# Optimization experiments

Hardware: AMD Instinct MI355X
Metric: run time of the kernel (lower is better)

Reference implementation:

```python
import jax, jax.numpy as jnp
import numpy as np

BN_SCALE = 1.0 / np.sqrt(1.0 + 1e-5)  # eval BatchNorm with running stats (0,1), gamma=1, beta=0


def fps(xyz, npoint):
    """Farthest point sampling. xyz: [B,N,3] -> int32 indices [B,npoint]. First pick is index 0 (as in pointnet2 CUDA)."""
    xyz = jax.lax.stop_gradient(xyz)  # output is integer indices; non-differentiable
    B, N, _ = xyz.shape

    def step(carry, _):
        dist, last = carry
        p = jnp.take_along_axis(xyz, last[:, None, None], axis=1)  # [B,1,3]
        d = jnp.sum((xyz - p) ** 2, axis=-1)                        # [B,N]
        dist = jnp.minimum(dist, d)
        nxt = jnp.argmax(dist, axis=-1).astype(jnp.int32)
        return (dist, nxt), nxt

    dist0 = jnp.full((B, N), 1e10, dtype=jnp.float32)
    first = jnp.zeros((B,), dtype=jnp.int32)
    _, rest = jax.lax.scan(step, (dist0, first), None, length=npoint - 1)  # [npoint-1, B]
    return jnp.concatenate([first[None, :], rest], axis=0).T  # [B, npoint]


def ball_query(xyz, new_xyz, radius, nsample):
    """For each center pick first nsample point indices with squared dist < radius^2; pad with first hit."""
    xyz = jax.lax.stop_gradient(xyz)
    new_xyz = jax.lax.stop_gradient(new_xyz)
    # expanded squared distance avoids materializing [B,S,N,3]
    d2 = (jnp.sum(new_xyz ** 2, -1)[:, :, None] + jnp.sum(xyz ** 2, -1)[:, None, :]
          - 2.0 * jnp.einsum('bsc,bnc->bsn', new_xyz, xyz))  # [B,S,N]
    N = xyz.shape[1]
    key = jnp.where(d2 < radius * radius, jnp.arange(N, dtype=jnp.int32)[None, None, :], N)
    idx = jnp.sort(key, axis=-1)[..., :nsample]          # first hits in index order
    return jnp.where(idx == N, idx[..., :1], idx)        # pad misses with first hit (center is always a hit)


_gather = jax.vmap(lambda p, i: p[i])  # points [N,C], idx [...] -> [..., C], batched over B


def _mlp(h, params):
    # pointwise Conv2d(1x1) + eval-BN + ReLU stack
    for w, b in params:
        h = jax.nn.relu((h @ w + b) * BN_SCALE)
    return h


def _sa(xyz, feats, npoint, nsample, radius, params):
    ci = fps(xyz, npoint)                               # [B,S]
    new_xyz = _gather(xyz, ci)                          # [B,S,3]
    idx = ball_query(xyz, new_xyz, radius, nsample)     # [B,S,K]
    gx = _gather(xyz, idx) - new_xyz[:, :, None, :]     # centered grouped xyz [B,S,K,3]
    h = jnp.concatenate([gx, _gather(feats, idx)], -1)  # [B,S,K,3+C]
    h = _mlp(h, params)
    return new_xyz, jnp.max(h, axis=2)                  # max-pool over neighbors -> [B,S,Cout]


def pointnetpp_forward(x, w1_0, b1_0, w1_1, b1_1, w1_2, b1_2,
                       w2_0, b2_0, w2_1, b2_1, w2_2, b2_2,
                       w3_0, b3_0, w3_1, b3_1, w3_2, b3_2, fc_w, fc_b):
    B0, NO, NP, C = x.shape
    pc = x.reshape(B0 * NO, NP, C)
    xyz, feats = pc[..., :3], pc[..., 3:]
    xyz, feats = _sa(xyz, feats, 32, 32, 0.2, [(w1_0, b1_0), (w1_1, b1_1), (w1_2, b1_2)])
    xyz, feats = _sa(xyz, feats, 16, 32, 0.4, [(w2_0, b2_0), (w2_1, b2_1), (w2_2, b2_2)])
    # group-all SA: no FPS, no centering (pointnet2 GroupAll)
    h = jnp.concatenate([xyz, feats], -1)[:, None]       # [B,1,N,3+C]
    h = _mlp(h, [(w3_0, b3_0), (w3_1, b3_1), (w3_2, b3_2)])
    g = jnp.max(h, axis=2).reshape(h.shape[0], -1)       # [B,768]
    out = g @ fc_w + fc_b                                # final Linear(768,768)
    return out.reshape(B0, NO, -1)                       # dropout = identity (eval / no_grad inference)


def setup_inputs():
    key = jax.random.key(0)
    ks = jax.random.split(key, 16)
    dims = {'w1_0': (6, 64), 'w1_1': (64, 64), 'w1_2': (64, 128),
            'w2_0': (131, 128), 'w2_1': (128, 128), 'w2_2': (128, 256),
            'w3_0': (259, 256), 'w3_1': (256, 512), 'w3_2': (512, 768),
            'fc_w': (768, 768)}
    inp = {'x': jax.random.normal(ks[0], (32, 64, 1024, 6), dtype=jnp.float32)}
    for i, (name, shp) in enumerate(dims.items()):
        inp[name] = 0.05 * jax.random.normal(ks[i + 1], shp, dtype=jnp.float32)
        bname = 'fc_b' if name == 'fc_w' else name.replace('w', 'b', 1)
        inp[bname] = jnp.zeros((shp[1],), dtype=jnp.float32)
    return inp


def reference(x, w1_0, b1_0, w1_1, b1_1, w1_2, b1_2,
              w2_0, b2_0, w2_1, b2_1, w2_2, b2_2,
              w3_0, b3_0, w3_1, b3_1, w3_2, b3_2, fc_w, fc_b):
    return pointnetpp_forward(x, w1_0, b1_0, w1_1, b1_1, w1_2, b1_2,
                              w2_0, b2_0, w2_1, b2_1, w2_2, b2_2,
                              w3_0, b3_0, w3_1, b3_1, w3_2, b3_2, fc_w, fc_b)
```

## Files before the change

### kernel.cpp

```cpp
#include <hip/hip_runtime.h>
#include <math.h>

#define BN_SCALE 0.999995000037499687f
#define NPTS 1024
#define NB   2048

typedef __attribute__((ext_vector_type(8))) short bh8;
typedef __attribute__((ext_vector_type(4))) float f32x4;

__device__ __forceinline__ float sq3(float x, float y, float z) {
  return __fadd_rn(__fadd_rn(__fmul_rn(x, x), __fmul_rn(y, y)), __fmul_rn(z, z));
}

__device__ __forceinline__ short bf16hi(float v) {
  unsigned u = __float_as_uint(v);
  unsigned r = (u + 0x7FFFu + ((u >> 16) & 1u)) >> 16;
  return (short)r;
}
__device__ __forceinline__ float bf16tof(short s) {
  unsigned u = ((unsigned)(unsigned short)s) << 16;
  return __uint_as_float(u);
}
__device__ __forceinline__ void bf16split(float v, short& hi, short& lo) {
  hi = bf16hi(v);
  lo = bf16hi(v - bf16tof(hi));
}

__global__ __launch_bounds__(256) void k_fps1(const float* __restrict__ x,
                                              float* __restrict__ nxyz1) {
  int b = blockIdx.x;
  const float* cloud = x + (size_t)b * NPTS * 6;
  __shared__ float px[NPTS], py[NPTS], pz[NPTS], dist[NPTS];
  __shared__ float wv_s[4];
  __shared__ int   wi_s[4];
  __shared__ int   last_s;
  int t = threadIdx.x;
  for (int i = t; i < NPTS; i += 256) {
    px[i] = cloud[i * 6 + 0];
    py[i] = cloud[i * 6 + 1];
    pz[i] = cloud[i * 6 + 2];
    dist[i] = 1e10f;
  }
  __syncthreads();
  if (t == 0) {
    nxyz1[(size_t)b * 96 + 0] = px[0];
    nxyz1[(size_t)b * 96 + 1] = py[0];
    nxyz1[(size_t)b * 96 + 2] = pz[0];
  }
  int last = 0;
  for (int s = 1; s < 32; ++s) {
    float lx = px[last], ly = py[last], lz = pz[last];
    float bv = -1.0f; int bi = NPTS;
    for (int i = t; i < NPTS; i += 256) {
      float dx = __fsub_rn(px[i], lx);
      float dy = __fsub_rn(py[i], ly);
      float dz = __fsub_rn(pz[i], lz);
      float d  = sq3(dx, dy, dz);
      float nd = fminf(dist[i], d);
      dist[i] = nd;
      if (nd > bv || (nd == bv && i < bi)) { bv = nd; bi = i; }
    }
    for (int off = 32; off; off >>= 1) {
      float ov = __shfl_down(bv, off);
      int   oi = __shfl_down(bi, off);
      if (ov > bv || (ov == bv && oi < bi)) { bv = ov; bi = oi; }
    }
    if ((t & 63) == 0) { wv_s[t >> 6] = bv; wi_s[t >> 6] = bi; }
    __syncthreads();
    if (t == 0) {
      for (int w = 1; w < 4; ++w)
        if (wv_s[w] > bv || (wv_s[w] == bv && wi_s[w] < bi)) { bv = wv_s[w]; bi = wi_s[w]; }
      last_s = bi;
      nxyz1[(size_t)b * 96 + s * 3 + 0] = px[bi];
      nxyz1[(size_t)b * 96 + s * 3 + 1] = py[bi];
      nxyz1[(size_t)b * 96 + s * 3 + 2] = pz[bi];
    }
    __syncthreads();
    last = last_s;
  }
}

__global__ __launch_bounds__(256) void k_bq1(const float* __restrict__ x,
                                             const float* __restrict__ nxyz1,
                                             int* __restrict__ idx1) {
  int c = blockIdx.x * 256 + threadIdx.x;
  if (c >= NB * 32) return;
  int b = c >> 5;
  const float* cloud = x + (size_t)b * NPTS * 6;
  float cx = nxyz1[c * 3 + 0], cy = nxyz1[c * 3 + 1], cz = nxyz1[c * 3 + 2];
  float sqc = sq3(cx, cy, cz);
  const float r2 = (float)(0.2 * 0.2);
  int hits = 0, fh = NPTS - 1;
  int* outp = idx1 + (size_t)c * 32;
  for (int i = 0; i < NPTS; ++i) {
    float ppx = cloud[i * 6 + 0], ppy = cloud[i * 6 + 1], ppz = cloud[i * 6 + 2];
    float sqp = sq3(ppx, ppy, ppz);
    float dt  = __fadd_rn(__fadd_rn(__fmul_rn(cx, ppx), __fmul_rn(cy, ppy)), __fmul_rn(cz, ppz));
    float d2  = __fsub_rn(__fadd_rn(sqc, sqp), __fmul_rn(2.0f, dt));
    if (d2 < r2) {
      if (hits == 0) fh = i;
      outp[hits] = i;
      if (++hits == 32) break;
    }
  }
  for (int j = hits; j < 32; ++j) outp[j] = fh;
}

__device__ __forceinline__ void prep_one(const float* __restrict__ src,
                                         short* __restrict__ dst,
                                         int q, int KT, int Kreal, int N) {
  int nt = q / (KT * 512);
  int r  = q - nt * (KT * 512);
  int kt = r >> 9;
  int e  = r & 511;
  int l = e >> 3, i = e & 7;
  int k = kt * 32 + ((l >> 4) << 3) + i;
  int col = nt * 16 + (l & 15);
  float v = (k < Kreal) ? src[(size_t)k * N + col] : 0.f;
  short hi, lo;
  bf16split(v, hi, lo);
  size_t base = ((size_t)(nt * KT + kt) * 2) * 512 + e;
  dst[base] = hi;
  dst[base + 512] = lo;
}

__global__ __launch_bounds__(256) void k_prep(const float* __restrict__ w0,
                                              const float* __restrict__ w1,
                                              const float* __restrict__ w2,
                                              short* __restrict__ wt0,
                                              short* __restrict__ wt1,
                                              short* __restrict__ wt2) {
  int p = blockIdx.x * 256 + threadIdx.x;
  const int S1 = 8 * 5 * 512, S2 = 8 * 4 * 512, S3 = 16 * 4 * 512;
  if (p < S1)                 prep_one(w0, wt0, p,           5, 131, 128);
  else if (p < S1 + S2)       prep_one(w1, wt1, p - S1,      4, 128, 128);
  else if (p < S1 + S2 + S3)  prep_one(w2, wt2, p - S1 - S2, 4, 128, 256);
}

__global__ __launch_bounds__(256) void k_prep1(const float* __restrict__ w0,
                                               const float* __restrict__ w1,
                                               const float* __restrict__ w2,
                                               short* __restrict__ wt0,
                                               short* __restrict__ wt1,
                                               short* __restrict__ wt2) {
  int p = blockIdx.x * 256 + threadIdx.x;
  const int S1 = 4 * 1 * 512, S2 = 4 * 2 * 512, S3 = 8 * 2 * 512;
  if (p < S1)                 prep_one(w0, wt0, p,           1, 6,  64);
  else if (p < S1 + S2)       prep_one(w1, wt1, p - S1,      2, 64, 64);
  else if (p < S1 + S2 + S3)  prep_one(w2, wt2, p - S1 - S2, 2, 64, 128);
}

__global__ __launch_bounds__(256) void k_prep3(const float* __restrict__ w0,
                                               const float* __restrict__ w1,
                                               const float* __restrict__ w2,
                                               const float* __restrict__ wf,
                                               short* __restrict__ wt0,
                                               short* __restrict__ wt1,
                                               short* __restrict__ wt2,
                                               short* __restrict__ wtf) {
  int p = blockIdx.x * 256 + threadIdx.x;
  const int S1 = 16 * 9 * 512;
  const int S2 = 32 * 8 * 512;
  const int S3 = 48 * 16 * 512;
  const int S4 = 48 * 24 * 512;
  if (p < S1)                      prep_one(w0, wt0, p,                9,  259, 256);
  else if (p < S1 + S2)            prep_one(w1, wt1, p - S1,           8,  256, 512);
  else if (p < S1 + S2 + S3)       prep_one(w2, wt2, p - S1 - S2,      16, 512, 768);
  else if (p < S1 + S2 + S3 + S4)  prep_one(wf, wtf, p - S1 - S2 - S3, 24, 768, 768);
}

template<int NTL, int KT, int PA, int MT>
__device__ __forceinline__ void mfma_gemm(const short* Ahi, const short* Alo,
                                          const short* __restrict__ wt,
                                          int w, int l, int lrow, int lk,
                                          f32x4 acc[][MT]) {
  for (int kt = 0; kt < KT; ++kt) {
    bh8 ahi[MT], alo[MT];
    #pragma unroll
    for (int mt = 0; mt < MT; ++mt) {
      int aoff = (mt * 16 + lrow) * PA + kt * 32 + lk;
      ahi[mt] = *(const bh8*)(Ahi + aoff);
      alo[mt] = *(const bh8*)(Alo + aoff);
    }
    #pragma unroll
    for (int ntl = 0; ntl < NTL; ++ntl) {
      int nt = w * NTL + ntl;
      bh8 bhi = *(const bh8*)(wt + (size_t)((nt * KT + kt) * 2 + 0) * 512 + l * 8);
      bh8 blo = *(const bh8*)(wt + (size_t)((nt * KT + kt) * 2 + 1) * 512 + l * 8);
      #pragma unroll
      for (int mt = 0; mt < MT; ++mt) {
        acc[ntl][mt] = __builtin_amdgcn_mfma_f32_16x16x32_bf16(ahi[mt], bhi, acc[ntl][mt], 0, 0, 0);
        acc[ntl][mt] = __builtin_amdgcn_mfma_f32_16x16x32_bf16(ahi[mt], blo, acc[ntl][mt], 0, 0, 0);
        acc[ntl][mt] = __builtin_amdgcn_mfma_f32_16x16x32_bf16(alo[mt], bhi, acc[ntl][mt], 0, 0, 0);
      }
    }
  }
}

template<int NTL, int PD, int MT>
__device__ __forceinline__ void epi_mid(f32x4 acc[][MT], const float* __restrict__ bias,
                                        short* Dhi, short* Dlo,
                                        int w, int lrow, int lhi4) {
  #pragma unroll
  for (int ntl = 0; ntl < NTL; ++ntl) {
    int col = (w * NTL + ntl) * 16 + lrow;
    float bv = bias[col];
    #pragma unroll
    for (int mt = 0; mt < MT; ++mt) {
      #pragma unroll
      for (int r = 0; r < 4; ++r) {
        int row = mt * 16 + lhi4 + r;
        float o = fmaxf((acc[ntl][mt][r] + bv) * BN_SCALE, 0.f);
        short hi, lo;
        bf16split(o, hi, lo);
        Dhi[row * PD + col] = hi;
        Dlo[row * PD + col] = lo;
      }
    }
  }
}

template<int NTL>
__device__ __forceinline__ void epi_max(f32x4 acc[][4], const float* __restrict__ bias,
                                        float* __restrict__ outA, float* __restrict__ outB,
                                        int w, int l, int lrow) {
  #pragma unroll
  for (int ntl = 0; ntl < NTL; ++ntl) {
    int col = (w * NTL + ntl) * 16 + lrow;
    float bv = bias[col];
    float m0 = 0.f, m1 = 0.f;
    #pragma unroll
    for (int mt = 0; mt < 4; ++mt) {
      float mm = 0.f;
      #pragma unroll
      for (int r = 0; r < 4; ++r)
        mm = fmaxf(mm, fmaxf((acc[ntl][mt][r] + bv) * BN_SCALE, 0.f));
      if (mt < 2) m0 = fmaxf(m0, mm); else m1 = fmaxf(m1, mm);
    }
    m0 = fmaxf(m0, __shfl_xor(m0, 16)); m0 = fmaxf(m0, __shfl_xor(m0, 32));
    m1 = fmaxf(m1, __shfl_xor(m1, 16)); m1 = fmaxf(m1, __shfl_xor(m1, 32));
    if (l < 16) {
      outA[col] = m0;
      outB[col] = m1;
    }
  }
}

__global__ __launch_bounds__(256) void k_sa1(const float* __restrict__ x,
                                             const float* __restrict__ nxyz1,
                                             const int* __restrict__ idx1,
                                             const short* __restrict__ wt0,
                                             const short* __restrict__ wt1,
                                             const short* __restrict__ wt2,
                                             const float* __restrict__ b0g,
                                             const float* __restrict__ b1g,
                                             const float* __restrict__ b2g,
                                             float* __restrict__ f1) {
  int c2 = blockIdx.x;
  int t  = threadIdx.x;
  __shared__ __align__(16) short lds[18432];
  __shared__ int pts[64];
  short* h0hi = lds;
  short* h0lo = lds + 4608;
  short* h1hi = lds + 9216;
  short* h1lo = lds + 13824;
  short* h2hi = lds;
  short* h2lo = lds + 4608;

  if (t < 64) {
    int g = t >> 5, samp = t & 31;
    pts[t] = idx1[(size_t)(c2 * 2 + g) * 32 + samp];
  }
  for (int j = t; j < 64 * 34; j += 256) {
    int s = j / 34, d = 6 + (j - s * 34);
    h0hi[s * 40 + d] = 0;
    h0lo[s * 40 + d] = 0;
  }
  __syncthreads();

  for (int j = t; j < 384; j += 256) {
    int s = j / 6, d = j - (j / 6) * 6;
    int g = s >> 5; int c = c2 * 2 + g; int b = c >> 5;
    int pt = pts[s];
    float v = x[((size_t)b * NPTS + pt) * 6 + d];
    if (d < 3) v -= nxyz1[(size_t)c * 3 + d];
    short hi, lo; bf16split(v, hi, lo);
    h0hi[s * 40 + d] = hi; h0lo[s * 40 + d] = lo;
  }
  __syncthreads();

  int l = t & 63, w = t >> 6;
  int lrow = l & 15;
  int lk   = (l >> 4) << 3;
  int lhi4 = (l >> 4) << 2;
  f32x4 zz = {0.f, 0.f, 0.f, 0.f};

  {
    f32x4 acc[1][4];
    #pragma unroll
    for (int j = 0; j < 4; ++j) acc[0][j] = zz;
    mfma_gemm<1, 1, 40, 4>(h0hi, h0lo, wt0, w, l, lrow, lk, acc);
    epi_mid<1, 72, 4>(acc, b0g, h1hi, h1lo, w, lrow, lhi4);
  }
  __syncthreads();
  {
    f32x4 acc[1][4];
    #pragma unroll
    for (int j = 0; j < 4; ++j) acc[0][j] = zz;
    mfma_gemm<1, 2, 72, 4>(h1hi, h1lo, wt1, w, l, lrow, lk, acc);
    epi_mid<1, 72, 4>(acc, b1g, h2hi, h2lo, w, lrow, lhi4);
  }
  __syncthreads();
  {
    f32x4 acc[2][4];
    #pragma unroll
    for (int i = 0; i < 2; ++i)
      #pragma unroll
      for (int j = 0; j < 4; ++j) acc[i][j] = zz;
    mfma_gemm<2, 2, 72, 4>(h2hi, h2lo, wt2, w, l, lrow, lk, acc);
    epi_max<2>(acc, b2g,
               f1 + (size_t)(c2 * 2 + 0) * 128,
               f1 + (size_t)(c2 * 2 + 1) * 128,
               w, l, lrow);
  }
}

__global__ __launch_bounds__(64) void k_fps2(const float* __restrict__ nxyz1,
                                             float* __restrict__ nxyz2) {
  int b = blockIdx.x;
  int t = threadIdx.x;
  const float* pts = nxyz1 + (size_t)b * 96;
  float ppx = 0.f, ppy = 0.f, ppz = 0.f, dist = -1.f;
  if (t < 32) { ppx = pts[t * 3]; ppy = pts[t * 3 + 1]; ppz = pts[t * 3 + 2]; dist = 1e10f; }
  if (t == 0) {
    nxyz2[(size_t)b * 48 + 0] = ppx;
    nxyz2[(size_t)b * 48 + 1] = ppy;
    nxyz2[(size_t)b * 48 + 2] = ppz;
  }
  int last = 0;
  for (int s = 1; s < 16; ++s) {
    float lx = __shfl(ppx, last), ly = __shfl(ppy, last), lz = __shfl(ppz, last);
    if (t < 32) {
      float dx = __fsub_rn(ppx, lx);
      float dy = __fsub_rn(ppy, ly);
      float dz = __fsub_rn(ppz, lz);
      dist = fminf(dist, sq3(dx, dy, dz));
    }
    float bv = dist; int bi = (t < 32) ? t : 1000;
    for (int off = 32; off; off >>= 1) {
      float ov = __shfl_xor(bv, off);
      int   oi = __shfl_xor(bi, off);
      if (ov > bv || (ov == bv && oi < bi)) { bv = ov; bi = oi; }
    }
    last = bi;
    float bx = __shfl(ppx, last), by = __shfl(ppy, last), bz = __shfl(ppz, last);
    if (t == 0) {
      nxyz2[(size_t)b * 48 + s * 3 + 0] = bx;
      nxyz2[(size_t)b * 48 + s * 3 + 1] = by;
      nxyz2[(size_t)b * 48 + s * 3 + 2] = bz;
    }
  }
}

__global__ __launch_bounds__(256) void k_bq2(const float* __restrict__ nxyz1,
                                             const float* __restrict__ nxyz2,
                                             int* __restrict__ idx2) {
  int c = blockIdx.x * 256 + threadIdx.x;
  if (c >= NB * 16) return;
  int b = c >> 4;
  const float* pts = nxyz1 + (size_t)b * 96;
  float cx = nxyz2[c * 3 + 0], cy = nxyz2[c * 3 + 1], cz = nxyz2[c * 3 + 2];
  float sqc = sq3(cx, cy, cz);
  const float r2 = (float)(0.4 * 0.4);
  int hits = 0, fh = 31;
  int* outp = idx2 + (size_t)c * 32;
  for (int i = 0; i < 32; ++i) {
    float ppx = pts[i * 3], ppy = pts[i * 3 + 1], ppz = pts[i * 3 + 2];
    float sqp = sq3(ppx, ppy, ppz);
    float dt  = __fadd_rn(__fadd_rn(__fmul_rn(cx, ppx), __fmul_rn(cy, ppy)), __fmul_rn(cz, ppz));
    float d2  = __fsub_rn(__fadd_rn(sqc, sqp), __fmul_rn(2.0f, dt));
    if (d2 < r2) { if (hits == 0) fh = i; outp[hits++] = i; }
  }
  for (int j = hits; j < 32; ++j) outp[j] = fh;
}

__global__ __launch_bounds__(256, 2) void k_sa2(const float* __restrict__ nxyz1,
                                                const float* __restrict__ nxyz2,
                                                const int* __restrict__ idx2,
                                                const float* __restrict__ f1,
                                                const short* __restrict__ wt0,
                                                const short* __restrict__ wt1,
                                                const short* __restrict__ wt2,
                                                const float* __restrict__ b0g,
                                                const float* __restrict__ b1g,
                                                const float* __restrict__ b2g,
                                                float* __restrict__ f2) {
  int c2 = blockIdx.x;
  int t  = threadIdx.x;
  __shared__ __align__(16) short lds[38912];
  __shared__ int pts[64];
  short* h0hi = lds;
  short* h0lo = lds + 10752;
  short* h1hi = lds + 21504;
  short* h1lo = lds + 30208;
  short* h2hi = lds;
  short* h2lo = lds + 10752;

  if (t < 64) {
    int g = t >> 5, samp = t & 31;
    pts[t] = idx2[(size_t)(c2 * 2 + g) * 32 + samp];
  }
  for (int j = t; j < 64 * 29; j += 256) {
    int s = j / 29, d = 131 + (j - s * 29);
    h0hi[s * 168 + d] = 0;
    h0lo[s * 168 + d] = 0;
  }
  __syncthreads();

  for (int j = t; j < 192; j += 256) {
    int s = j / 3, d = j - (j / 3) * 3;
    int g = s >> 5; int c = c2 * 2 + g; int b = c >> 4;
    int pt = pts[s];
    float v = nxyz1[((size_t)b * 32 + pt) * 3 + d] - nxyz2[(size_t)c * 3 + d];
    short hi, lo; bf16split(v, hi, lo);
    h0hi[s * 168 + d] = hi; h0lo[s * 168 + d] = lo;
  }
  for (int j = t; j < 2048; j += 256) {
    int s = j >> 5, d4 = j & 31;
    int g = s >> 5; int c = c2 * 2 + g; int b = c >> 4;
    int pt = pts[s];
    const float4 v4 = *reinterpret_cast<const float4*>(&f1[((size_t)b * 32 + pt) * 128 + d4 * 4]);
    int base = s * 168 + 3 + d4 * 4;
    short hi, lo;
    bf16split(v4.x, hi, lo); h0hi[base + 0] = hi; h0lo[base + 0] = lo;
    bf16split(v4.y, hi, lo); h0hi[base + 1] = hi; h0lo[base + 1] = lo;
    bf16split(v4.z, hi, lo); h0hi[base + 2] = hi; h0lo[base + 2] = lo;
    bf16split(v4.w, hi, lo); h0hi[base + 3] = hi; h0lo[base + 3] = lo;
  }
  __syncthreads();

  int l = t & 63, w = t >> 6;
  int lrow = l & 15;
  int lk   = (l >> 4) << 3;
  int lhi4 = (l >> 4) << 2;
  f32x4 zz = {0.f, 0.f, 0.f, 0.f};

  {
    f32x4 acc[2][4];
    #pragma unroll
    for (int i = 0; i < 2; ++i)
      #pragma unroll
      for (int j = 0; j < 4; ++j) acc[i][j] = zz;
    mfma_gemm<2, 5, 168, 4>(h0hi, h0lo, wt0, w, l, lrow, lk, acc);
    epi_mid<2, 136, 4>(acc, b0g, h1hi, h1lo, w, lrow, lhi4);
  }
  __syncthreads();
  {
    f32x4 acc[2][4];
    #pragma unroll
    for (int i = 0; i < 2; ++i)
      #pragma unroll
      for (int j = 0; j < 4; ++j) acc[i][j] = zz;
    mfma_gemm<2, 4, 136, 4>(h1hi, h1lo, wt1, w, l, lrow, lk, acc);
    epi_mid<2, 136, 4>(acc, b1g, h2hi, h2lo, w, lrow, lhi4);
  }
  __syncthreads();
  {
    f32x4 acc[4][4];
    #pragma unroll
    for (int i = 0; i < 4; ++i)
      #pragma unroll
      for (int j = 0; j < 4; ++j) acc[i][j] = zz;
    mfma_gemm<4, 4, 136, 4>(h2hi, h2lo, wt2, w, l, lrow, lk, acc);
    epi_max<4>(acc, b2g,
               f2 + (size_t)(c2 * 2 + 0) * 256,
               f2 + (size_t)(c2 * 2 + 1) * 256,
               w, l, lrow);
  }
}

__global__ __launch_bounds__(256) void k_mlp3(const float* __restrict__ nxyz2,
                                              const float* __restrict__ f2,
                                              const short* __restrict__ wt0,
                                              const short* __restrict__ wt1,
                                              const short* __restrict__ wt2,
                                              const float* __restrict__ b0g,
                                              const float* __restrict__ b1g,
                                              const float* __restrict__ b2g,
                                              short* __restrict__ ghi,
                                              short* __restrict__ glo) {
  int b = blockIdx.x;
  int t = threadIdx.x;
  __shared__ __align__(16) short lds[25088];
  short* h1hi = lds;
  short* h1lo = lds + 4224;
  short* h0hi = lds + 8448;
  short* h0lo = lds + 13184;
  short* h2hi = lds + 8448;
  short* h2lo = lds + 16768;

  for (int j = t; j < 16 * 29; j += 256) {
    int s = j / 29, d = 259 + (j - s * 29);
    h0hi[s * 296 + d] = 0;
    h0lo[s * 296 + d] = 0;
  }
  for (int j = t; j < 16 * 259; j += 256) {
    int s = j / 259, d = j - s * 259;
    float v = (d < 3) ? nxyz2[(size_t)b * 48 + s * 3 + d]
                      : f2[((size_t)b * 16 + s) * 256 + (d - 3)];
    short hi, lo; bf16split(v, hi, lo);
    h0hi[s * 296 + d] = hi;
    h0lo[s * 296 + d] = lo;
  }
  __syncthreads();

  int l = t & 63, w = t >> 6;
  int lrow = l & 15;
  int lk   = (l >> 4) << 3;
  int lhi4 = (l >> 4) << 2;
  f32x4 zz = {0.f, 0.f, 0.f, 0.f};

  {
    f32x4 acc[4][1];
    #pragma unroll
    for (int i = 0; i < 4; ++i) acc[i][0] = zz;
    mfma_gemm<4, 9, 296, 1>(h0hi, h0lo, wt0, w, l, lrow, lk, acc);
    epi_mid<4, 264, 1>(acc, b0g, h1hi, h1lo, w, lrow, lhi4);
  }
  __syncthreads();
  {
    f32x4 acc[8][1];
    #pragma unroll
    for (int i = 0; i < 8; ++i) acc[i][0] = zz;
    mfma_gemm<8, 8, 264, 1>(h1hi, h1lo, wt1, w, l, lrow, lk, acc);
    epi_mid<8, 520, 1>(acc, b1g, h2hi, h2lo, w, lrow, lhi4);
  }
  __syncthreads();
  {
    f32x4 acc[12][1];
    #pragma unroll
    for (int i = 0; i < 12; ++i) acc[i][0] = zz;
    mfma_gemm<12, 16, 520, 1>(h2hi, h2lo, wt2, w, l, lrow, lk, acc);
    #pragma unroll
    for (int ntl = 0; ntl < 12; ++ntl) {
      int col = (w * 12 + ntl) * 16 + lrow;
      float bv = b2g[col];
      float m = 0.f;
      #pragma unroll
      for (int r = 0; r < 4; ++r)
        m = fmaxf(m, fmaxf((acc[ntl][0][r] + bv) * BN_SCALE, 0.f));
      m = fmaxf(m, __shfl_xor(m, 16));
      m = fmaxf(m, __shfl_xor(m, 32));
      if (l < 16) {
        short hi, lo; bf16split(m, hi, lo);
        ghi[(size_t)b * 768 + col] = hi;
        glo[(size_t)b * 768 + col] = lo;
      }
    }
  }
}

__global__ __launch_bounds__(256) void k_fc(const short* __restrict__ ghi,
                                            const short* __restrict__ glo,
                                            const short* __restrict__ wtf,
                                            const float* __restrict__ fcb,
                                            float* __restrict__ outp) {
  int mblk = blockIdx.x;
  int nh   = blockIdx.y;
  int t = threadIdx.x;
  int l = t & 63, w = t >> 6;
  int lrow = l & 15;
  int lk   = (l >> 4) << 3;
  int lhi4 = (l >> 4) << 2;
  f32x4 zz = {0.f, 0.f, 0.f, 0.f};

  const short* Ahi = ghi + (size_t)mblk * 16 * 768;
  const short* Alo = glo + (size_t)mblk * 16 * 768;
  const short* wt  = wtf + (size_t)nh * 24 * 24 * 1024;

  f32x4 acc[6][1];
  #pragma unroll
  for (int i = 0; i < 6; ++i) acc[i][0] = zz;
  mfma_gemm<6, 24, 768, 1>(Ahi, Alo, wt, w, l, lrow, lk, acc);

  #pragma unroll
  for (int ntl = 0; ntl < 6; ++ntl) {
    int col = nh * 384 + (w * 6 + ntl) * 16 + lrow;
    float bv = fcb[col];
    #pragma unroll
    for (int r = 0; r < 4; ++r) {
      int row = mblk * 16 + lhi4 + r;
      outp[(size_t)row * 768 + col] = acc[ntl][0][r] + bv;
    }
  }
}

extern "C" void kernel_launch(void* const* d_in, const int* in_sizes, int n_in,
                              void* d_out, int out_size, void* d_ws, size_t ws_size,
                              hipStream_t stream) {
  const float* x    = (const float*)d_in[0];
  const float* w1_0 = (const float*)d_in[1];  const float* b1_0 = (const float*)d_in[2];
  const float* w1_1 = (const float*)d_in[3];  const float* b1_1 = (const float*)d_in[4];
  const float* w1_2 = (const float*)d_in[5];  const float* b1_2 = (const float*)d_in[6];
  const float* w2_0 = (const float*)d_in[7];  const float* b2_0 = (const float*)d_in[8];
  const float* w2_1 = (const float*)d_in[9];  const float* b2_1 = (const float*)d_in[10];
  const float* w2_2 = (const float*)d_in[11]; const float* b2_2 = (const float*)d_in[12];
  const float* w3_0 = (const float*)d_in[13]; const float* b3_0 = (const float*)d_in[14];
  const float* w3_1 = (const float*)d_in[15]; const float* b3_1 = (const float*)d_in[16];
  const float* w3_2 = (const float*)d_in[17]; const float* b3_2 = (const float*)d_in[18];
  const float* fc_w = (const float*)d_in[19]; const float* fc_b = (const float*)d_in[20];
  float* outp = (float*)d_out;

  const size_t n_float = (size_t)NB * 96 + (size_t)NB * 48 +
                         (size_t)NB * 32 * 128 + (size_t)NB * 16 * 256;
  const size_t n_int   = (size_t)NB * 32 * 32 + (size_t)NB * 16 * 32;
  const size_t n_short = (40960 + 32768 + 65536) + (4096 + 8192 + 16384) +
                         (147456 + 262144 + 786432) + 1179648 +
                         2 * (size_t)NB * 768;
  const size_t need_bytes = n_float * 4 + n_int * 4 + n_short * 2;
  if (ws_size < need_bytes) return;

  float* nxyz1 = (float*)d_ws;
  float* nxyz2 = nxyz1 + (size_t)NB * 96;
  float* f1    = nxyz2 + (size_t)NB * 48;
  float* f2    = f1    + (size_t)NB * 32 * 128;
  int*   idx1  = (int*)(f2 + (size_t)NB * 16 * 256);
  int*   idx2  = idx1 + (size_t)NB * 32 * 32;
  short* wt0   = (short*)(idx2 + (size_t)NB * 16 * 32);
  short* wt1   = wt0 + 40960;
  short* wt2   = wt1 + 32768;
  short* wt10  = wt2 + 65536;
  short* wt11  = wt10 + 4096;
  short* wt12  = wt11 + 8192;
  short* wt30  = wt12 + 16384;
  short* wt31  = wt30 + 147456;
  short* wt32  = wt31 + 262144;
  short* wtfc  = wt32 + 786432;
  short* ghi   = wtfc + 1179648;
  short* glo   = ghi + (size_t)NB * 768;

  k_prep <<<272, 256, 0, stream>>>(w2_0, w2_1, w2_2, wt0, wt1, wt2);
  k_prep1<<<56, 256, 0, stream>>>(w1_0, w1_1, w1_2, wt10, wt11, wt12);
  k_prep3<<<4640, 256, 0, stream>>>(w3_0, w3_1, w3_2, fc_w, wt30, wt31, wt32, wtfc);
  k_fps1<<<NB, 256, 0, stream>>>(x, nxyz1);
  k_bq1 <<<(NB * 32) / 256, 256, 0, stream>>>(x, nxyz1, idx1);
  k_sa1 <<<NB * 16, 256, 0, stream>>>(x, nxyz1, idx1, wt10, wt11, wt12,
                                      b1_0, b1_1, b1_2, f1);
  k_fps2<<<NB, 64, 0, stream>>>(nxyz1, nxyz2);
  k_bq2 <<<(NB * 16) / 256, 256, 0, stream>>>(nxyz1, nxyz2, idx2);
  k_sa2 <<<NB * 8, 256, 0, stream>>>(nxyz1, nxyz2, idx2, f1, wt0, wt1, wt2,
                                     b2_0, b2_1, b2_2, f2);
  k_mlp3<<<NB, 256, 0, stream>>>(nxyz2, f2, wt30, wt31, wt32,
                                 b3_0, b3_1, b3_2, ghi, glo);
  k_fc  <<<dim3(NB / 16, 2), 256, 0, stream>>>(ghi, glo, wtfc, fc_b, outp);
}
```

Baseline: 1.506 ms.

## Store intermediate features as split bf16 and widen SA2 blocks to 512 threads

SA1 and SA2 now write their max-pooled features already split into bf16 hi/lo planes instead of fp32. The consumers (SA2 and MLP3) can then copy them into LDS with 16-byte vector loads and skip the per-element conversion. The input channel order is permuted so features come first and xyz offsets last, keeping the vector copies aligned, and the weight prep remaps rows to match. SA2 also moves from 256 to 512 threads per block, so each wave computes fewer output tiles; the tradeoff is higher register and occupancy pressure from __launch_bounds__(512,4).

Measured after the change: 1.286 ms. -14.6%, faster.

```diff
diff --git a/kernel.cpp b/kernel.cpp
--- a/kernel.cpp
+++ b/kernel.cpp
@@ -108,7 +108,7 @@
 
 __device__ __forceinline__ void prep_one(const float* __restrict__ src,
                                          short* __restrict__ dst,
-                                         int q, int KT, int Kreal, int N) {
+                                         int q, int KT, int Kreal, int N, int permS) {
   int nt = q / (KT * 512);
   int r  = q - nt * (KT * 512);
   int kt = r >> 9;
@@ -116,7 +116,9 @@
   int l = e >> 3, i = e & 7;
   int k = kt * 32 + ((l >> 4) << 3) + i;
   int col = nt * 16 + (l & 15);
-  float v = (k < Kreal) ? src[(size_t)k * N + col] : 0.f;
+  int ko = k;
+  if (permS) ko = (k < permS) ? k + 3 : k - permS;
+  float v = (k < Kreal) ? src[(size_t)ko * N + col] : 0.f;
   short hi, lo;
   bf16split(v, hi, lo);
   size_t base = ((size_t)(nt * KT + kt) * 2) * 512 + e;
@@ -132,9 +134,9 @@
                                               short* __restrict__ wt2) {
   int p = blockIdx.x * 256 + threadIdx.x;
   const int S1 = 8 * 5 * 512, S2 = 8 * 4 * 512, S3 = 16 * 4 * 512;
-  if (p < S1)                 prep_one(w0, wt0, p,           5, 131, 128);
-  else if (p < S1 + S2)       prep_one(w1, wt1, p - S1,      4, 128, 128);
-  else if (p < S1 + S2 + S3)  prep_one(w2, wt2, p - S1 - S2, 4, 128, 256);
+  if (p < S1)                 prep_one(w0, wt0, p,           5, 131, 128, 128);
+  else if (p < S1 + S2)       prep_one(w1, wt1, p - S1,      4, 128, 128, 0);
+  else if (p < S1 + S2 + S3)  prep_one(w2, wt2, p - S1 - S2, 4, 128, 256, 0);
 }
 
 __global__ __launch_bounds__(256) void k_prep1(const float* __restrict__ w0,
@@ -145,9 +147,9 @@
                                                short* __restrict__ wt2) {
   int p = blockIdx.x * 256 + threadIdx.x;
   const int S1 = 4 * 1 * 512, S2 = 4 * 2 * 512, S3 = 8 * 2 * 512;
-  if (p < S1)                 prep_one(w0, wt0, p,           1, 6,  64);
-  else if (p < S1 + S2)       prep_one(w1, wt1, p - S1,      2, 64, 64);
-  else if (p < S1 + S2 + S3)  prep_one(w2, wt2, p - S1 - S2, 2, 64, 128);
+  if (p < S1)                 prep_one(w0, wt0, p,           1, 6,  64, 0);
+  else if (p < S1 + S2)       prep_one(w1, wt1, p - S1,      2, 64, 64, 0);
+  else if (p < S1 + S2 + S3)  prep_one(w2, wt2, p - S1 - S2, 2, 64, 128, 0);
 }
 
 __global__ __launch_bounds__(256) void k_prep3(const float* __restrict__ w0,
@@ -163,10 +165,10 @@
   const int S2 = 32 * 8 * 512;
   const int S3 = 48 * 16 * 512;
   const int S4 = 48 * 24 * 512;
-  if (p < S1)                      prep_one(w0, wt0, p,                9,  259, 256);
-  else if (p < S1 + S2)            prep_one(w1, wt1, p - S1,           8,  256, 512);
-  else if (p < S1 + S2 + S3)       prep_one(w2, wt2, p - S1 - S2,      16, 512, 768);
-  else if (p < S1 + S2 + S3 + S4)  prep_one(wf, wtf, p - S1 - S2 - S3, 24, 768, 768);
+  if (p < S1)                      prep_one(w0, wt0, p,                9,  259, 256, 256);
+  else if (p < S1 + S2)            prep_one(w1, wt1, p - S1,           8,  256, 512, 0);
+  else if (p < S1 + S2 + S3)       prep_one(w2, wt2, p - S1 - S2,      16, 512, 768, 0);
+  else if (p < S1 + S2 + S3 + S4)  prep_one(wf, wtf, p - S1 - S2 - S3, 24, 768, 768, 0);
 }
 
 template<int NTL, int KT, int PA, int MT>
@@ -221,9 +223,10 @@
 }
 
 template<int NTL>
-__device__ __forceinline__ void epi_max(f32x4 acc[][4], const float* __restrict__ bias,
-                                        float* __restrict__ outA, float* __restrict__ outB,
-                                        int w, int l, int lrow) {
+__device__ __forceinline__ void epi_max_bf(f32x4 acc[][4], const float* __restrict__ bias,
+                                           short* __restrict__ hiA, short* __restrict__ loA,
+                                           short* __restrict__ hiB, short* __restrict__ loB,
+                                           int w, int l, int lrow) {
   #pragma unroll
   for (int ntl = 0; ntl < NTL; ++ntl) {
     int col = (w * NTL + ntl) * 16 + lrow;
@@ -240,8 +243,9 @@
     m0 = fmaxf(m0, __shfl_xor(m0, 16)); m0 = fmaxf(m0, __shfl_xor(m0, 32));
     m1 = fmaxf(m1, __shfl_xor(m1, 16)); m1 = fmaxf(m1, __shfl_xor(m1, 32));
     if (l < 16) {
-      outA[col] = m0;
-      outB[col] = m1;
+      short hi, lo;
+      bf16split(m0, hi, lo); hiA[col] = hi; loA[col] = lo;
+      bf16split(m1, hi, lo); hiB[col] = hi; loB[col] = lo;
     }
   }
 }
@@ -255,7 +259,8 @@
                                              const float* __restrict__ b0g,
                                              const float* __restrict__ b1g,
                                              const float* __restrict__ b2g,
-                                             float* __restrict__ f1) {
+                                             short* __restrict__ f1hi,
+                                             short* __restrict__ f1lo) {
   int c2 = blockIdx.x;
   int t  = threadIdx.x;
   __shared__ __align__(16) short lds[18432];
@@ -318,10 +323,10 @@
       #pragma unroll
       for (int j = 0; j < 4; ++j) acc[i][j] = zz;
     mfma_gemm<2, 2, 72, 4>(h2hi, h2lo, wt2, w, l, lrow, lk, acc);
-    epi_max<2>(acc, b2g,
-               f1 + (size_t)(c2 * 2 + 0) * 128,
-               f1 + (size_t)(c2 * 2 + 1) * 128,
-               w, l, lrow);
+    epi_max_bf<2>(acc, b2g,
+                  f1hi + (size_t)(c2 * 2 + 0) * 128, f1lo + (size_t)(c2 * 2 + 0) * 128,
+                  f1hi + (size_t)(c2 * 2 + 1) * 128, f1lo + (size_t)(c2 * 2 + 1) * 128,
+                  w, l, lrow);
   }
 }
 
@@ -384,17 +389,19 @@
   for (int j = hits; j < 32; ++j) outp[j] = fh;
 }
 
-__global__ __launch_bounds__(256, 2) void k_sa2(const float* __restrict__ nxyz1,
+__global__ __launch_bounds__(512, 4) void k_sa2(const float* __restrict__ nxyz1,
                                                 const float* __restrict__ nxyz2,
                                                 const int* __restrict__ idx2,
-                                                const float* __restrict__ f1,
+                                                const short* __restrict__ f1hi,
+                                                const short* __restrict__ f1lo,
                                                 const short* __restrict__ wt0,
                                                 const short* __restrict__ wt1,
                                                 const short* __restrict__ wt2,
                                                 const float* __restrict__ b0g,
                                                 const float* __restrict__ b1g,
                                                 const float* __restrict__ b2g,
-                                                float* __restrict__ f2) {
+                                                short* __restrict__ f2hi,
+                                                short* __restrict__ f2lo) {
   int c2 = blockIdx.x;
   int t  = threadIdx.x;
   __shared__ __align__(16) short lds[38912];
@@ -410,32 +417,28 @@
     int g = t >> 5, samp = t & 31;
     pts[t] = idx2[(size_t)(c2 * 2 + g) * 32 + samp];
   }
-  for (int j = t; j < 64 * 29; j += 256) {
+  for (int j = t; j < 64 * 29; j += 512) {
     int s = j / 29, d = 131 + (j - s * 29);
     h0hi[s * 168 + d] = 0;
     h0lo[s * 168 + d] = 0;
   }
   __syncthreads();
 
-  for (int j = t; j < 192; j += 256) {
+  for (int j = t; j < 1024; j += 512) {
+    int s = j >> 4, c8 = j & 15;
+    int g = s >> 5; int c = c2 * 2 + g; int b = c >> 4;
+    int pt = pts[s];
+    size_t src = ((size_t)b * 32 + pt) * 128 + c8 * 8;
+    *(bh8*)(h0hi + s * 168 + c8 * 8) = *(const bh8*)(f1hi + src);
+    *(bh8*)(h0lo + s * 168 + c8 * 8) = *(const bh8*)(f1lo + src);
+  }
+  for (int j = t; j < 192; j += 512) {
     int s = j / 3, d = j - (j / 3) * 3;
     int g = s >> 5; int c = c2 * 2 + g; int b = c >> 4;
     int pt = pts[s];
     float v = nxyz1[((size_t)b * 32 + pt) * 3 + d] - nxyz2[(size_t)c * 3 + d];
     short hi, lo; bf16split(v, hi, lo);
-    h0hi[s * 168 + d] = hi; h0lo[s * 168 + d] = lo;
-  }
-  for (int j = t; j < 2048; j += 256) {
-    int s = j >> 5, d4 = j & 31;
-    int g = s >> 5; int c = c2 * 2 + g; int b = c >> 4;
-    int pt = pts[s];
-    const float4 v4 = *reinterpret_cast<const float4*>(&f1[((size_t)b * 32 + pt) * 128 + d4 * 4]);
-    int base = s * 168 + 3 + d4 * 4;
-    short hi, lo;
-    bf16split(v4.x, hi, lo); h0hi[base + 0] = hi; h0lo[base + 0] = lo;
-    bf16split(v4.y, hi, lo); h0hi[base + 1] = hi; h0lo[base + 1] = lo;
-    bf16split(v4.z, hi, lo); h0hi[base + 2] = hi; h0lo[base + 2] = lo;
-    bf16split(v4.w, hi, lo); h0hi[base + 3] = hi; h0lo[base + 3] = lo;
+    h0hi[s * 168 + 128 + d] = hi; h0lo[s * 168 + 128 + d] = lo;
   }
   __syncthreads();
 
@@ -446,41 +449,38 @@
   f32x4 zz = {0.f, 0.f, 0.f, 0.f};
 
   {
+    f32x4 acc[1][4];
+    #pragma unroll
+    for (int j = 0; j < 4; ++j) acc[0][j] = zz;
+    mfma_gemm<1, 5, 168, 4>(h0hi, h0lo, wt0, w, l, lrow, lk, acc);
+    epi_mid<1, 136, 4>(acc, b0g, h1hi, h1lo, w, lrow, lhi4);
+  }
+  __syncthreads();
+  {
+    f32x4 acc[1][4];
+    #pragma unroll
+    for (int j = 0; j < 4; ++j) acc[0][j] = zz;
+    mfma_gemm<1, 4, 136, 4>(h1hi, h1lo, wt1, w, l, lrow, lk, acc);
+    epi_mid<1, 136, 4>(acc, b1g, h2hi, h2lo, w, lrow, lhi4);
+  }
+  __syncthreads();
+  {
     f32x4 acc[2][4];
     #pragma unroll
     for (int i = 0; i < 2; ++i)
       #pragma unroll
       for (int j = 0; j < 4; ++j) acc[i][j] = zz;
-    mfma_gemm<2, 5, 168, 4>(h0hi, h0lo, wt0, w, l, lrow, lk, acc);
-    epi_mid<2, 136, 4>(acc, b0g, h1hi, h1lo, w, lrow, lhi4);
-  }
-  __syncthreads();
-  {
-    f32x4 acc[2][4];
-    #pragma unroll
-    for (int i = 0; i < 2; ++i)
-      #pragma unroll
-      for (int j = 0; j < 4; ++j) acc[i][j] = zz;
-    mfma_gemm<2, 4, 136, 4>(h1hi, h1lo, wt1, w, l, lrow, lk, acc);
-    epi_mid<2, 136, 4>(acc, b1g, h2hi, h2lo, w, lrow, lhi4);
-  }
-  __syncthreads();
-  {
-    f32x4 acc[4][4];
-    #pragma unroll
-    for (int i = 0; i < 4; ++i)
-      #pragma unroll
-      for (int j = 0; j < 4; ++j) acc[i][j] = zz;
-    mfma_gemm<4, 4, 136, 4>(h2hi, h2lo, wt2, w, l, lrow, lk, acc);
-    epi_max<4>(acc, b2g,
-               f2 + (size_t)(c2 * 2 + 0) * 256,
-               f2 + (size_t)(c2 * 2 + 1) * 256,
-               w, l, lrow);
+    mfma_gemm<2, 4, 136, 4>(h2hi, h2lo, wt2, w, l, lrow, lk, acc);
+    epi_max_bf<2>(acc, b2g,
+                  f2hi + (size_t)(c2 * 2 + 0) * 256, f2lo + (size_t)(c2 * 2 + 0) * 256,
+                  f2hi + (size_t)(c2 * 2 + 1) * 256, f2lo + (size_t)(c2 * 2 + 1) * 256,
+                  w, l, lrow);
   }
 }
 
 __global__ __launch_bounds__(256) void k_mlp3(const float* __restrict__ nxyz2,
-                                              const float* __restrict__ f2,
+                                              const short* __restrict__ f2hi,
+                                              const short* __restrict__ f2lo,
                                               const short* __restrict__ wt0,
                                               const short* __restrict__ wt1,
                                               const short* __restrict__ wt2,
@@ -504,13 +504,18 @@
     h0hi[s * 296 + d] = 0;
     h0lo[s * 296 + d] = 0;
   }
-  for (int j = t; j < 16 * 259; j += 256) {
-    int s = j / 259, d = j - s * 259;
-    float v = (d < 3) ? nxyz2[(size_t)b * 48 + s * 3 + d]
-                      : f2[((size_t)b * 16 + s) * 256 + (d - 3)];
+  for (int j = t; j < 512; j += 256) {
+    int s = j >> 5, c8 = j & 31;
+    size_t src = ((size_t)b * 16 + s) * 256 + c8 * 8;
+    *(bh8*)(h0hi + s * 296 + c8 * 8) = *(const bh8*)(f2hi + src);
+    *(bh8*)(h0lo + s * 296 + c8 * 8) = *(const bh8*)(f2lo + src);
+  }
+  for (int j = t; j < 48; j += 256) {
+    int s = j / 3, d = j - (j / 3) * 3;
+    float v = nxyz2[(size_t)b * 48 + s * 3 + d];
     short hi, lo; bf16split(v, hi, lo);
-    h0hi[s * 296 + d] = hi;
-    h0lo[s * 296 + d] = lo;
+    h0hi[s * 296 + 256 + d] = hi;
+    h0lo[s * 296 + 256 + d] = lo;
   }
   __syncthreads();
 
@@ -611,22 +616,25 @@
   const float* fc_w = (const float*)d_in[19]; const float* fc_b = (const float*)d_in[20];
   float* outp = (float*)d_out;
 
-  const size_t n_float = (size_t)NB * 96 + (size_t)NB * 48 +
-                         (size_t)NB * 32 * 128 + (size_t)NB * 16 * 256;
-  const size_t n_int   = (size_t)NB * 32 * 32 + (size_t)NB * 16 * 32;
-  const size_t n_short = (40960 + 32768 + 65536) + (4096 + 8192 + 16384) +
-                         (147456 + 262144 + 786432) + 1179648 +
-                         2 * (size_t)NB * 768;
+  const size_t n_float = (size_t)NB * 96 + (size_t)NB * 48;
+  const size_t n_int   = (size_t)NB * 1024 + (size_t)NB * 512;
+  const size_t n_short = 4 * (size_t)NB * 4096
+                       + (40960 + 32768 + 65536)
+                       + (4096 + 8192 + 16384)
+                       + (147456 + 262144 + 786432) + 1179648
+                       + 2 * (size_t)NB * 768;
   const size_t need_bytes = n_float * 4 + n_int * 4 + n_short * 2;
   if (ws_size < need_bytes) return;
 
   float* nxyz1 = (float*)d_ws;
   float* nxyz2 = nxyz1 + (size_t)NB * 96;
-  float* f1    = nxyz2 + (size_t)NB * 48;
-  float* f2    = f1    + (size_t)NB * 32 * 128;
-  int*   idx1  = (int*)(f2 + (size_t)NB * 16 * 256);
-  int*   idx2  = idx1 + (size_t)NB * 32 * 32;
-  short* wt0   = (short*)(idx2 + (size_t)NB * 16 * 32);
+  int*   idx1  = (int*)(nxyz2 + (size_t)NB * 48);
+  int*   idx2  = idx1 + (size_t)NB * 1024;
+  short* f1hi  = (short*)(idx2 + (size_t)NB * 512);
+  short* f1lo  = f1hi + (size_t)NB * 4096;
+  short* f2hi  = f1lo + (size_t)NB * 4096;
+  short* f2lo  = f2hi + (size_t)NB * 4096;
+  short* wt0   = f2lo + (size_t)NB * 4096;
   short* wt1   = wt0 + 40960;
   short* wt2   = wt1 + 32768;
   short* wt10  = wt2 + 65536;
@@ -645,12 +653,12 @@
   k_fps1<<<NB, 256, 0, stream>>>(x, nxyz1);
   k_bq1 <<<(NB * 32) / 256, 256, 0, stream>>>(x, nxyz1, idx1);
   k_sa1 <<<NB * 16, 256, 0, stream>>>(x, nxyz1, idx1, wt10, wt11, wt12,
-                                      b1_0, b1_1, b1_2, f1);
+                                      b1_0, b1_1, b1_2, f1hi, f1lo);
   k_fps2<<<NB, 64, 0, stream>>>(nxyz1, nxyz2);
   k_bq2 <<<(NB * 16) / 256, 256, 0, stream>>>(nxyz1, nxyz2, idx2);
-  k_sa2 <<<NB * 8, 256, 0, stream>>>(nxyz1, nxyz2, idx2, f1, wt0, wt1, wt2,
-                                     b2_0, b2_1, b2_2, f2);
-  k_mlp3<<<NB, 256, 0, stream>>>(nxyz2, f2, wt30, wt31, wt32,
+  k_sa2 <<<NB * 8, 512, 0, stream>>>(nxyz1, nxyz2, idx2, f1hi, f1lo,
+                                     wt0, wt1, wt2, b2_0, b2_1, b2_2, f2hi, f2lo);
+  k_mlp3<<<NB, 256, 0, stream>>>(nxyz2, f2hi, f2lo, wt30, wt31, wt32,
                                  b3_0, b3_1, b3_2, ghi, glo);
   k_fc  <<<dim3(NB / 16, 2), 256, 0, stream>>>(ghi, glo, wtfc, fc_b, outp);
 }
```
